# Performance work log

Hardware: AMD Instinct MI355X
Metric: run time of the kernel (lower is better)

The kernel has to match this reference:

```python
import jax, jax.numpy as jnp
import numpy as np

N_NODES = 50000
N_EDGES = 800000
D_IN = 128
D_HID = 128
D_OUT = 128


def _graph_conv(x, src, dst, ew, w_rel, w_root, b):
    # PyG GraphConv: out_i = (sum_{j->i} ew_ji * x_j) @ w_rel.T + b + x_i @ w_root.T
    msg = x[src] * ew[:, None]                                   # [E, F] gather + scale
    agg = jax.ops.segment_sum(msg, dst, num_segments=x.shape[0])  # [N, F] scatter-add
    return agg @ w_rel.T + x @ w_root.T + b


def setup_inputs() -> dict:
    key = jax.random.key(0)
    ks = jax.random.split(key, 12)
    s = 0.05
    x = jax.random.normal(ks[0], (N_NODES, D_IN), dtype=jnp.float32)
    edge_index = jax.random.randint(ks[1], (2, N_EDGES), 0, N_NODES, dtype=jnp.int32)
    edge_weight = jax.random.uniform(ks[2], (N_EDGES,), dtype=jnp.float32)
    return {
        "x": x,
        "edge_index": edge_index,
        "edge_weight": edge_weight,
        "w1_rel": jax.random.normal(ks[3], (D_HID, D_IN), dtype=jnp.float32) * s,
        "w1_root": jax.random.normal(ks[4], (D_HID, D_IN), dtype=jnp.float32) * s,
        "b1": jnp.zeros((D_HID,), dtype=jnp.float32),
        "w2_rel": jax.random.normal(ks[5], (D_HID, D_HID), dtype=jnp.float32) * s,
        "w2_root": jax.random.normal(ks[6], (D_HID, D_HID), dtype=jnp.float32) * s,
        "b2": jnp.zeros((D_HID,), dtype=jnp.float32),
        "w3_rel": jax.random.normal(ks[7], (D_OUT, D_HID), dtype=jnp.float32) * s,
        "w3_root": jax.random.normal(ks[8], (D_OUT, D_HID), dtype=jnp.float32) * s,
        "b3": jnp.zeros((D_OUT,), dtype=jnp.float32),
    }


def reference(x, edge_index, edge_weight,
              w1_rel, w1_root, b1,
              w2_rel, w2_root, b2,
              w3_rel, w3_root, b3):
    src, dst = edge_index[0], edge_index[1]
    h = _graph_conv(x, src, dst, edge_weight, w1_rel, w1_root, b1)
    h = jax.nn.relu(h)  # dropout is identity in eval mode
    h = _graph_conv(h, src, dst, edge_weight, w2_rel, w2_root, b2)
    h = jax.nn.relu(h)
    out = _graph_conv(h, src, dst, edge_weight, w3_rel, w3_root, b3)
    return out
```

## Files before the change

### kernel.cpp

```cpp
#include <hip/hip_runtime.h>
#include <hip/hip_bf16.h>

#define DFEAT   128
#define BCAP    2048
#define NB_MAX  1024

typedef __attribute__((ext_vector_type(8))) short bf16x8;
typedef __attribute__((ext_vector_type(4))) float f32x4;
typedef unsigned int uint;


__global__ __launch_bounds__(1024) void bin_scatter(const int* __restrict__ src,
                                                    const int* __restrict__ dst,
                                                    const float* __restrict__ ew,
                                                    int* __restrict__ cursor,
                                                    int2* __restrict__ bedges,
                                                    int E, int NB) {
    __shared__ int hist[NB_MAX];
    __shared__ int base[NB_MAX];
    const int tid = threadIdx.x;
    for (int b = tid; b < NB; b += 1024) hist[b] = 0;
    __syncthreads();

    int  s[8]; float w[8]; int bk[8]; int dl[8];
    const int i0 = blockIdx.x * 8192 + tid;
    #pragma unroll
    for (int k = 0; k < 8; ++k) {
        int i = i0 + k * 1024;
        if (i < E) {
            s[k] = src[i]; w[k] = ew[i];
            int d = dst[i];
            bk[k] = d >> 6; dl[k] = d & 63;
            atomicAdd(&hist[bk[k]], 1);
        } else bk[k] = -1;
    }
    __syncthreads();
    for (int b = tid; b < NB; b += 1024) {
        int c = hist[b];
        base[b] = (c > 0) ? atomicAdd(&cursor[b], c) : 0;
        hist[b] = 0;
    }
    __syncthreads();
    #pragma unroll
    for (int k = 0; k < 8; ++k) {
        if (bk[k] >= 0) {
            int r = atomicAdd(&hist[bk[k]], 1);
            int pos = base[bk[k]] + r;
            if (pos < ((bk[k] + 1) << 11)) {
                bedges[pos] = make_int2(s[k] | (dl[k] << 26), __float_as_int(w[k]));
            }
        }
    }
}


__global__ __launch_bounds__(1024) void bucket_sort(const int* __restrict__ cursor,
                                                    int2* __restrict__ bedges,
                                                    int* __restrict__ rowptr,
                                                    int* __restrict__ rowend, int N) {
    __shared__ int2 buf[BCAP];
    __shared__ int hist[64], pref[64], rank[64];
    const int b = blockIdx.x, tid = threadIdx.x;
    const int base = b << 11;
    const int cnt = cursor[b] - base;

    if (tid < 64) hist[tid] = 0;
    __syncthreads();
    for (int i = tid; i < cnt; i += 1024) {
        int2 e = bedges[base + i];
        buf[i] = e;
        atomicAdd(&hist[((uint)e.x) >> 26], 1);
    }
    __syncthreads();
    if (tid < 64) {
        int v = hist[tid];
        int s = v;
        #pragma unroll
        for (int off = 1; off < 64; off <<= 1) {
            int t = __shfl_up(s, off, 64);
            if (tid >= off) s += t;
        }
        pref[tid] = s - v;
        rank[tid] = 0;
        int node = b * 64 + tid;
        if (node < N) {
            rowptr[node] = base + (s - v);
            rowend[node] = base + s;
        }
    }
    __syncthreads();
    for (int i = tid; i < cnt; i += 1024) {
        int2 e = buf[i];
        int dl = ((uint)e.x) >> 26;
        int r = atomicAdd(&rank[dl], 1);
        bedges[base + pref[dl] + r] = e;
    }
}


__device__ __forceinline__ uint pack_bf16x2(float a, float b) {
    __hip_bfloat16 ba = __float2bfloat16(a);
    __hip_bfloat16 bb = __float2bfloat16(b);
    unsigned short ua = *(unsigned short*)&ba;
    unsigned short ub = *(unsigned short*)&bb;
    return (uint)ua | ((uint)ub << 16);
}

__device__ __forceinline__ void fma8(float* acc, uint4 q, float wt) {
    acc[0] = fmaf(wt, __uint_as_float(q.x << 16),         acc[0]);
    acc[1] = fmaf(wt, __uint_as_float(q.x & 0xffff0000u), acc[1]);
    acc[2] = fmaf(wt, __uint_as_float(q.y << 16),         acc[2]);
    acc[3] = fmaf(wt, __uint_as_float(q.y & 0xffff0000u), acc[3]);
    acc[4] = fmaf(wt, __uint_as_float(q.z << 16),         acc[4]);
    acc[5] = fmaf(wt, __uint_as_float(q.z & 0xffff0000u), acc[5]);
    acc[6] = fmaf(wt, __uint_as_float(q.w << 16),         acc[6]);
    acc[7] = fmaf(wt, __uint_as_float(q.w & 0xffff0000u), acc[7]);
}


__global__ void prep_all(const float* __restrict__ x, uint* __restrict__ xb, int n2,
                         const float* __restrict__ w1r, const float* __restrict__ w1t,
                         const float* __restrict__ w2r, const float* __restrict__ w2t,
                         const float* __restrict__ w3r, const float* __restrict__ w3t,
                         __hip_bfloat16* __restrict__ Bp1, __hip_bfloat16* __restrict__ Bp2,
                         __hip_bfloat16* __restrict__ Bp3,
                         int* __restrict__ cursor, int NB, int cvtB) {
    const int b = blockIdx.x, tid = threadIdx.x;
    if (b < cvtB) {
        int i = b * 256 + tid;
        if (i < n2) {
            float2 v = ((const float2*)x)[i];
            xb[i] = pack_bf16x2(v.x, v.y);
        }
    } else if (b < cvtB + 384) {
        const int b2 = b - cvtB;
        const int g = b2 >> 7;
        const int idx = (b2 & 127) * 256 + tid;
        const float* wrel  = (g == 0) ? w1r : (g == 1) ? w2r : w3r;
        const float* wroot = (g == 0) ? w1t : (g == 1) ? w2t : w3t;
        __hip_bfloat16* Bp = (g == 0) ? Bp1 : (g == 1) ? Bp2 : Bp3;
        int j     = idx & 7;
        int lane  = (idx >> 3) & 63;
        int nfrag = (idx >> 9) & 7;
        int kstep = idx >> 12;
        int k = kstep * 32 + (lane >> 4) * 8 + j;
        int n = nfrag * 16 + (lane & 15);
        float v = (k < 128) ? wrel[n * 128 + k] : wroot[n * 128 + (k - 128)];
        Bp[idx] = __float2bfloat16(v);
    } else {
        int i = (b - cvtB - 384) * 256 + tid;
        if (i < NB) cursor[i] = i * BCAP;
    }
}


template<int RELU, int OUTF32>
__global__ __launch_bounds__(512) void fused_layer(const uint* __restrict__ f,
                                                   const int* __restrict__ rowptr,
                                                   const int* __restrict__ rowend,
                                                   const int2* __restrict__ bedges,
                                                   const bf16x8* __restrict__ Bp,
                                                   const float* __restrict__ bias,
                                                   float* __restrict__ outf,
                                                   __hip_bfloat16* __restrict__ outb,
                                                   int N) {
    __shared__ uint4 As4[32][17];
    const int tid  = threadIdx.x;
    const int lane = tid & 63, wid = tid >> 6;
    const int grp  = lane >> 4;
    const int sub  = lane & 15;
    const int tile = blockIdx.x * 32;
    const uint4* f4 = (const uint4*)f;

    const int pn = tile + wid * 4 + (lane & 3);
    int rp = 0, re = 0;
    if (lane < 4 && pn < N) { rp = rowptr[pn]; re = rowend[pn]; }

    int begC = __builtin_amdgcn_readlane(rp, 0);
    int degC = __builtin_amdgcn_readlane(re, 0) - begC;
    int2 eCur = make_int2(0, 0);
    if (degC > 0) eCur = bedges[begC + min(lane, min(degC, 64) - 1)];

    for (int qn = 0; qn < 4; ++qn) {
        const int beg = begC, deg = degC;
        int2 eNext = make_int2(0, 0);
        if (qn < 3) {
            begC = __builtin_amdgcn_readlane(rp, qn + 1);
            degC = __builtin_amdgcn_readlane(re, qn + 1) - begC;
            if (degC > 0) eNext = bedges[begC + min(lane, min(degC, 64) - 1)];
        }

        float acc[8];
        #pragma unroll
        for (int i = 0; i < 8; ++i) acc[i] = 0.f;

        int done = 0;
        int2 e = eCur;
        while (done < deg) {
            const int chunk = min(deg - done, 64);
            if (done) e = bedges[beg + done + min(lane, chunk - 1)];
            const int vsrc = e.x & 0x03FFFFFF;
            const int vwb  = (lane < chunk) ? e.y : 0;
            const int iters = (chunk + 7) & ~7;
            int   s0 = __shfl(vsrc, grp, 64);
            float w0 = __int_as_float(__shfl(vwb, grp, 64));
            int   s1 = __shfl(vsrc, 4 + grp, 64);
            float w1 = __int_as_float(__shfl(vwb, 4 + grp, 64));
            uint4 q0 = f4[(size_t)s0 * 16 + sub];
            uint4 q1 = f4[(size_t)s1 * 16 + sub];
            for (int j = 8; j < iters; j += 8) {
                int   s2 = __shfl(vsrc, j + grp, 64);
                float w2 = __int_as_float(__shfl(vwb, j + grp, 64));
                int   s3 = __shfl(vsrc, j + 4 + grp, 64);
                float w3 = __int_as_float(__shfl(vwb, j + 4 + grp, 64));
                uint4 q2 = f4[(size_t)s2 * 16 + sub];
                uint4 q3 = f4[(size_t)s3 * 16 + sub];
                fma8(acc, q0, w0); fma8(acc, q1, w1);
                q0 = q2; q1 = q3; w0 = w2; w1 = w3;
            }
            fma8(acc, q0, w0); fma8(acc, q1, w1);
            done += chunk;
        }

        #pragma unroll
        for (int i = 0; i < 8; ++i) {
            acc[i] += __shfl_xor(acc[i], 16, 64);
            acc[i] += __shfl_xor(acc[i], 32, 64);
        }
        if (lane < 16) {
            uint4 o;
            o.x = pack_bf16x2(acc[0], acc[1]);
            o.y = pack_bf16x2(acc[2], acc[3]);
            o.z = pack_bf16x2(acc[4], acc[5]);
            o.w = pack_bf16x2(acc[6], acc[7]);
            As4[wid * 4 + qn][sub] = o;
        }
        eCur = eNext;
    }
    __syncthreads();

    const int wr = wid >> 2, wc = wid & 3;
    const int lrow = lane & 15;
    const int lkq  = (lane >> 4);
    const short* As_s = (const short*)&As4[0][0];
    const short* fb   = (const short*)f;

    int gr = tile + wr * 16 + lrow;
    if (gr >= N) gr = N - 1;

    f32x4 acc2[2];
    acc2[0] = (f32x4){0.f, 0.f, 0.f, 0.f};
    acc2[1] = (f32x4){0.f, 0.f, 0.f, 0.f};

    #pragma unroll
    for (int ks = 0; ks < 8; ++ks) {
        bf16x8 a;
        if (ks < 4)
            a = *(const bf16x8*)(As_s + (wr * 16 + lrow) * 136 + ks * 32 + lkq * 8);
        else
            a = *(const bf16x8*)(fb + (size_t)gr * 128 + (ks - 4) * 32 + lkq * 8);
        #pragma unroll
        for (int nf = 0; nf < 2; ++nf) {
            bf16x8 b = Bp[(ks * 8 + (wc * 2 + nf)) * 64 + lane];
            acc2[nf] = __builtin_amdgcn_mfma_f32_16x16x32_bf16(a, b, acc2[nf], 0, 0, 0);
        }
    }

    const int crow = (lane >> 4) * 4;
    const int ccol = lane & 15;
    #pragma unroll
    for (int nf = 0; nf < 2; ++nf) {
        const int col = wc * 32 + nf * 16 + ccol;
        const float bv = bias[col];
        #pragma unroll
        for (int r = 0; r < 4; ++r) {
            const int row = tile + wr * 16 + crow + r;
            if (row < N) {
                float v = acc2[nf][r] + bv;
                if (RELU) v = fmaxf(v, 0.f);
                if (OUTF32) outf[(size_t)row * 128 + col] = v;
                else        outb[(size_t)row * 128 + col] = __float2bfloat16(v);
            }
        }
    }
}


extern "C" void kernel_launch(void* const* d_in, const int* in_sizes, int n_in,
                              void* d_out, int out_size, void* d_ws, size_t ws_size,
                              hipStream_t stream) {
    const float* x   = (const float*)d_in[0];
    const int*  eidx = (const int*)d_in[1];
    const float* ew  = (const float*)d_in[2];
    const float* w1r = (const float*)d_in[3];
    const float* w1t = (const float*)d_in[4];
    const float* b1  = (const float*)d_in[5];
    const float* w2r = (const float*)d_in[6];
    const float* w2t = (const float*)d_in[7];
    const float* b2  = (const float*)d_in[8];
    const float* w3r = (const float*)d_in[9];
    const float* w3t = (const float*)d_in[10];
    const float* b3  = (const float*)d_in[11];
    float* out = (float*)d_out;

    const int N  = in_sizes[0] / DFEAT;
    const int E  = in_sizes[2];
    const int NB = (N + 63) / 64;

    char* ws = (char*)d_ws;
    size_t off = 0;
    auto alloc = [&](size_t bytes) -> void* {
        off = (off + 255) & ~(size_t)255;
        void* p = ws + off;
        off += bytes;
        return p;
    };
    int*  cursor = (int*)alloc((size_t)NB * 4);
    int*  rowptr = (int*)alloc((size_t)N * 4);
    int*  rowend = (int*)alloc((size_t)N * 4);
    int2* bedges = (int2*)alloc((size_t)NB * BCAP * 8);
    __hip_bfloat16* Bp1 = (__hip_bfloat16*)alloc(32768 * 2);
    __hip_bfloat16* Bp2 = (__hip_bfloat16*)alloc(32768 * 2);
    __hip_bfloat16* Bp3 = (__hip_bfloat16*)alloc(32768 * 2);
    uint* xb   = (uint*)alloc((size_t)N * 64 * 4);
    uint* h1b  = (uint*)alloc((size_t)N * 64 * 4);
    uint* h2b  = (uint*)alloc((size_t)N * 64 * 4);
    (void)ws_size;

    const int* src = eidx;
    const int* dst = eidx + E;

    const int n2 = N * 64;
    const int cvtB = (n2 + 255) / 256;
    const int curB = (NB + 255) / 256;
    prep_all<<<cvtB + 384 + curB, 256, 0, stream>>>(x, xb, n2,
                                                    w1r, w1t, w2r, w2t, w3r, w3t,
                                                    Bp1, Bp2, Bp3, cursor, NB, cvtB);

    bin_scatter<<<(E + 8191) / 8192, 1024, 0, stream>>>(src, dst, ew, cursor, bedges, E, NB);
    bucket_sort<<<NB, 1024, 0, stream>>>(cursor, bedges, rowptr, rowend, N);

    const int NB2 = (N + 31) / 32;
    fused_layer<1, 0><<<NB2, 512, 0, stream>>>(xb, rowptr, rowend, bedges, (const bf16x8*)Bp1,
                                               b1, nullptr, (__hip_bfloat16*)h1b, N);
    fused_layer<1, 0><<<NB2, 512, 0, stream>>>(h1b, rowptr, rowend, bedges, (const bf16x8*)Bp2,
                                               b2, nullptr, (__hip_bfloat16*)h2b, N);
    fused_layer<0, 1><<<NB2, 512, 0, stream>>>(h2b, rowptr, rowend, bedges, (const bf16x8*)Bp3,
                                               b3, out, nullptr, N);
}
```

Before: 156.3 us.

## Double fused layer tile to 64 nodes with 2x2 MFMA register tiling

Each block now aggregates 64 destination nodes (8 per wave) instead of 32, and each wave computes a 32x32 output sub-tile with a 2x2 set of MFMA accumulators. Each B-fragment load is reused across two row fragments, and per-block overhead is spread over more nodes. In exchange the grid halves to the bucket count, reducing parallelism and lengthening the serial per-wave gather loop, and register pressure rises.

```diff
diff --git a/kernel.cpp b/kernel.cpp
--- a/kernel.cpp
+++ b/kernel.cpp
@@ -164,27 +164,27 @@
                                                    float* __restrict__ outf,
                                                    __hip_bfloat16* __restrict__ outb,
                                                    int N) {
-    __shared__ uint4 As4[32][17];
+    __shared__ uint4 As4[64][17];
     const int tid  = threadIdx.x;
     const int lane = tid & 63, wid = tid >> 6;
     const int grp  = lane >> 4;
     const int sub  = lane & 15;
-    const int tile = blockIdx.x * 32;
+    const int tile = blockIdx.x * 64;
     const uint4* f4 = (const uint4*)f;
 
-    const int pn = tile + wid * 4 + (lane & 3);
+    const int pn = tile + wid * 8 + (lane & 7);
     int rp = 0, re = 0;
-    if (lane < 4 && pn < N) { rp = rowptr[pn]; re = rowend[pn]; }
+    if (lane < 8 && pn < N) { rp = rowptr[pn]; re = rowend[pn]; }
 
     int begC = __builtin_amdgcn_readlane(rp, 0);
     int degC = __builtin_amdgcn_readlane(re, 0) - begC;
     int2 eCur = make_int2(0, 0);
     if (degC > 0) eCur = bedges[begC + min(lane, min(degC, 64) - 1)];
 
-    for (int qn = 0; qn < 4; ++qn) {
+    for (int qn = 0; qn < 8; ++qn) {
         const int beg = begC, deg = degC;
         int2 eNext = make_int2(0, 0);
-        if (qn < 3) {
+        if (qn < 7) {
             begC = __builtin_amdgcn_readlane(rp, qn + 1);
             degC = __builtin_amdgcn_readlane(re, qn + 1) - begC;
             if (degC > 0) eNext = bedges[begC + min(lane, min(degC, 64) - 1)];
@@ -233,7 +233,7 @@
             o.y = pack_bf16x2(acc[2], acc[3]);
             o.z = pack_bf16x2(acc[4], acc[5]);
             o.w = pack_bf16x2(acc[6], acc[7]);
-            As4[wid * 4 + qn][sub] = o;
+            As4[wid * 8 + qn][sub] = o;
         }
         eCur = eNext;
     }
@@ -245,41 +245,56 @@
     const short* As_s = (const short*)&As4[0][0];
     const short* fb   = (const short*)f;
 
-    int gr = tile + wr * 16 + lrow;
-    if (gr >= N) gr = N - 1;
-
-    f32x4 acc2[2];
-    acc2[0] = (f32x4){0.f, 0.f, 0.f, 0.f};
-    acc2[1] = (f32x4){0.f, 0.f, 0.f, 0.f};
+    int grow[2];
+    #pragma unroll
+    for (int mi = 0; mi < 2; ++mi) {
+        int r = tile + wr * 32 + mi * 16 + lrow;
+        grow[mi] = (r < N) ? r : (N - 1);
+    }
+
+    f32x4 acc2[2][2];
+    #pragma unroll
+    for (int mi = 0; mi < 2; ++mi)
+        #pragma unroll
+        for (int nf = 0; nf < 2; ++nf) acc2[mi][nf] = (f32x4){0.f, 0.f, 0.f, 0.f};
 
     #pragma unroll
     for (int ks = 0; ks < 8; ++ks) {
-        bf16x8 a;
-        if (ks < 4)
-            a = *(const bf16x8*)(As_s + (wr * 16 + lrow) * 136 + ks * 32 + lkq * 8);
-        else
-            a = *(const bf16x8*)(fb + (size_t)gr * 128 + (ks - 4) * 32 + lkq * 8);
-        #pragma unroll
-        for (int nf = 0; nf < 2; ++nf) {
-            bf16x8 b = Bp[(ks * 8 + (wc * 2 + nf)) * 64 + lane];
-            acc2[nf] = __builtin_amdgcn_mfma_f32_16x16x32_bf16(a, b, acc2[nf], 0, 0, 0);
-        }
+        bf16x8 a[2], b[2];
+        #pragma unroll
+        for (int mi = 0; mi < 2; ++mi) {
+            if (ks < 4)
+                a[mi] = *(const bf16x8*)(As_s + (wr * 32 + mi * 16 + lrow) * 136 + ks * 32 + lkq * 8);
+            else
+                a[mi] = *(const bf16x8*)(fb + (size_t)grow[mi] * 128 + (ks - 4) * 32 + lkq * 8);
+        }
+        #pragma unroll
+        for (int nf = 0; nf < 2; ++nf)
+            b[nf] = Bp[(ks * 8 + (wc * 2 + nf)) * 64 + lane];
+        #pragma unroll
+        for (int mi = 0; mi < 2; ++mi)
+            #pragma unroll
+            for (int nf = 0; nf < 2; ++nf)
+                acc2[mi][nf] = __builtin_amdgcn_mfma_f32_16x16x32_bf16(a[mi], b[nf], acc2[mi][nf], 0, 0, 0);
     }
 
     const int crow = (lane >> 4) * 4;
     const int ccol = lane & 15;
     #pragma unroll
-    for (int nf = 0; nf < 2; ++nf) {
-        const int col = wc * 32 + nf * 16 + ccol;
-        const float bv = bias[col];
-        #pragma unroll
-        for (int r = 0; r < 4; ++r) {
-            const int row = tile + wr * 16 + crow + r;
-            if (row < N) {
-                float v = acc2[nf][r] + bv;
-                if (RELU) v = fmaxf(v, 0.f);
-                if (OUTF32) outf[(size_t)row * 128 + col] = v;
-                else        outb[(size_t)row * 128 + col] = __float2bfloat16(v);
+    for (int mi = 0; mi < 2; ++mi) {
+        #pragma unroll
+        for (int nf = 0; nf < 2; ++nf) {
+            const int col = wc * 32 + nf * 16 + ccol;
+            const float bv = bias[col];
+            #pragma unroll
+            for (int r = 0; r < 4; ++r) {
+                const int row = tile + wr * 32 + mi * 16 + crow + r;
+                if (row < N) {
+                    float v = acc2[mi][nf][r] + bv;
+                    if (RELU) v = fmaxf(v, 0.f);
+                    if (OUTF32) outf[(size_t)row * 128 + col] = v;
+                    else        outb[(size_t)row * 128 + col] = __float2bfloat16(v);
+                }
             }
         }
     }
@@ -340,11 +355,10 @@
     bin_scatter<<<(E + 8191) / 8192, 1024, 0, stream>>>(src, dst, ew, cursor, bedges, E, NB);
     bucket_sort<<<NB, 1024, 0, stream>>>(cursor, bedges, rowptr, rowend, N);
 
-    const int NB2 = (N + 31) / 32;
-    fused_layer<1, 0><<<NB2, 512, 0, stream>>>(xb, rowptr, rowend, bedges, (const bf16x8*)Bp1,
-                                               b1, nullptr, (__hip_bfloat16*)h1b, N);
-    fused_layer<1, 0><<<NB2, 512, 0, stream>>>(h1b, rowptr, rowend, bedges, (const bf16x8*)Bp2,
-                                               b2, nullptr, (__hip_bfloat16*)h2b, N);
-    fused_layer<0, 1><<<NB2, 512, 0, stream>>>(h2b, rowptr, rowend, bedges, (const bf16x8*)Bp3,
-                                               b3, out, nullptr, N);
-}
+    fused_layer<1, 0><<<NB, 512, 0, stream>>>(xb, rowptr, rowend, bedges, (const bf16x8*)Bp1,
+                                              b1, nullptr, (__hip_bfloat16*)h1b, N);
+    fused_layer<1, 0><<<NB, 512, 0, stream>>>(h1b, rowptr, rowend, bedges, (const bf16x8*)Bp2,
+                                              b2, nullptr, (__hip_bfloat16*)h2b, N);
+    fused_layer<0, 1><<<NB, 512, 0, stream>>>(h2b, rowptr, rowend, bedges, (const bf16x8*)Bp3,
+                                              b3, out, nullptr, N);
+}
```

New measurement: 151.4 us, median of 2. 1.03x faster.
